# Performance work log

Measured on AMD Instinct MI355X. Metric: run time of the kernel, lower is better.

Reference implementation:

```python
import jax, jax.numpy as jnp
import numpy as np

# Multi-scale feature pyramid (static: determines per-level slice bounds)
SPATIAL_SHAPES = np.array([[100, 100], [50, 50], [25, 25], [13, 13], [7, 7]])  # (H, W) per level
LEVEL_START = np.concatenate([[0], np.cumsum(SPATIAL_SHAPES[:, 0] * SPATIAL_SHAPES[:, 1])])[:-1]
C = 256       # hidden_inplanes
HEADS = 8     # head_nums
POINTS = 4    # point_nums
LEVELS = 5    # feature_level_nums
FF = 2048     # feedforward_planes
DH = C // HEADS


def setup_inputs() -> dict:
    key = jax.random.key(0)
    ks = jax.random.split(key, 16)
    B = 2
    L = int((SPATIAL_SHAPES[:, 0] * SPATIAL_SHAPES[:, 1]).sum())  # 13343 tokens
    s = 0.02
    return {
        'src': jax.random.normal(ks[0], (B, L, C), jnp.float32),
        'pos': jax.random.normal(ks[1], (B, L, C), jnp.float32) * 0.1,
        'reference_points': jax.random.uniform(ks[2], (B, L, LEVELS, 2), jnp.float32),
        'wv': jax.random.normal(ks[3], (C, C), jnp.float32) * s,
        'bv': jnp.zeros((C,), jnp.float32),
        'wo': jax.random.normal(ks[4], (C, HEADS * LEVELS * POINTS * 2), jnp.float32) * s,
        'bo': jax.random.normal(ks[5], (HEADS * LEVELS * POINTS * 2,), jnp.float32) * 0.5,
        'wa': jax.random.normal(ks[6], (C, HEADS * LEVELS * POINTS), jnp.float32) * s,
        'ba': jnp.zeros((HEADS * LEVELS * POINTS,), jnp.float32),
        'wout': jax.random.normal(ks[7], (C, C), jnp.float32) * s,
        'bout': jnp.zeros((C,), jnp.float32),
        'ln1g': jnp.ones((C,), jnp.float32),
        'ln1b': jnp.zeros((C,), jnp.float32),
        'w1': jax.random.normal(ks[8], (C, FF), jnp.float32) * s,
        'b1': jnp.zeros((FF,), jnp.float32),
        'w2': jax.random.normal(ks[9], (FF, C), jnp.float32) * s,
        'b2': jnp.zeros((C,), jnp.float32),
        'ln2g': jnp.ones((C,), jnp.float32),
        'ln2b': jnp.zeros((C,), jnp.float32),
    }


def layernorm(x, g, b, eps=1e-5):
    m = jnp.mean(x, -1, keepdims=True)
    v = jnp.var(x, -1, keepdims=True)
    return (x - m) * jax.lax.rsqrt(v + eps) * g + b


def bilinear_sample(val, loc, Hs, Ws):
    # val: [B, heads, H*W, dh]   loc: [B, heads, Lq, P, 2] normalized coords in [0,1]
    # grid_sample semantics, align_corners=False, zero padding outside
    px = loc[..., 0] * Ws - 0.5
    py = loc[..., 1] * Hs - 0.5
    x0 = jnp.floor(px); y0 = jnp.floor(py)
    lx = px - x0;       ly = py - y0
    x0i = x0.astype(jnp.int32); y0i = y0.astype(jnp.int32)
    gather = jax.vmap(jax.vmap(lambda v, i: v[i]))  # over batch, head dims
    out = jnp.zeros(loc.shape[:-1] + (val.shape[-1],), val.dtype)
    for dx, dy, w in ((0, 0, (1 - lx) * (1 - ly)), (1, 0, lx * (1 - ly)),
                      (0, 1, (1 - lx) * ly), (1, 1, lx * ly)):
        xi = x0i + dx; yi = y0i + dy
        valid = (xi >= 0) & (xi < Ws) & (yi >= 0) & (yi < Hs)
        idx = jnp.clip(yi, 0, Hs - 1) * Ws + jnp.clip(xi, 0, Ws - 1)
        g = gather(val, idx)  # [B, heads, Lq, P, dh]
        out = out + (w * valid)[..., None] * g
    return out


def msdeform_attn(query, value_in, ref, wv, bv, wo, bo, wa, ba, wout, bout):
    B, Lq, _ = query.shape
    # value projection -> [B, heads, Len, dh]
    value = (value_in @ wv + bv).reshape(B, -1, HEADS, DH).transpose(0, 2, 1, 3)
    offsets = (query @ wo + bo).reshape(B, Lq, HEADS, LEVELS, POINTS, 2)
    attn = jax.nn.softmax((query @ wa + ba).reshape(B, Lq, HEADS, LEVELS * POINTS), -1)
    attn = attn.reshape(B, Lq, HEADS, LEVELS, POINTS)
    # offset normalizer = (W, H) per level
    norml = jnp.asarray(SPATIAL_SHAPES[:, ::-1].copy(), jnp.float32)
    loc = ref[:, :, None, :, None, :] + offsets / norml[None, None, None, :, None, :]
    acc = jnp.zeros((B, Lq, HEADS, DH), query.dtype)
    for l in range(LEVELS):
        Hs, Ws = int(SPATIAL_SHAPES[l, 0]), int(SPATIAL_SHAPES[l, 1])
        s = int(LEVEL_START[l])
        vl = value[:, :, s:s + Hs * Ws, :]
        locl = jnp.transpose(loc[:, :, :, l], (0, 2, 1, 3, 4))  # [B, heads, Lq, P, 2]
        samp = bilinear_sample(vl, locl, Hs, Ws)                 # [B, heads, Lq, P, dh]
        acc = acc + jnp.einsum('bhqpd,bqhp->bqhd', samp, attn[:, :, :, l])
    return acc.reshape(B, Lq, C) @ wout + bout


def reference(src, pos, reference_points, wv, bv, wo, bo, wa, ba, wout, bout,
              ln1g, ln1b, w1, b1, w2, b2, ln2g, ln2b):
    # DeformableTransformerEncoderLayer (eval mode, dropout off)
    q = src + pos
    src2 = msdeform_attn(q, src, reference_points, wv, bv, wo, bo, wa, ba, wout, bout)
    x = layernorm(src + src2, ln1g, ln1b)
    ffn = jax.nn.relu(x @ w1 + b1) @ w2 + b2
    return layernorm(x + ffn, ln2g, ln2b)
```

## Files before the change

### kernel.cpp

```cpp
#include <hip/hip_runtime.h>
#include <hip/hip_bf16.h>

typedef __hip_bfloat16 bf16;
typedef unsigned short ushort_t;
typedef __attribute__((ext_vector_type(8))) short bf16x8;
typedef __attribute__((ext_vector_type(16))) float f32x16;

__device__ __forceinline__ float us2f(unsigned short u) {
    unsigned int x = ((unsigned int)u) << 16;
    return __uint_as_float(x);
}
__device__ __forceinline__ ushort_t f2us(float f) {
    return ((__hip_bfloat16_raw)__float2bfloat16(f)).x;
}

__device__ __forceinline__ void gl_lds16(const ushort_t* g, ushort_t* l) {
    __builtin_amdgcn_global_load_lds(
        (const __attribute__((address_space(1))) void*)g,
        (__attribute__((address_space(3))) void*)l, 16, 0, 0);
}

__global__ __launch_bounds__(256) void cast2_kernel(
    const float* __restrict__ src, const float* __restrict__ pos,
    bf16* __restrict__ src_b, bf16* __restrict__ q_b, int n)
{
    int i = (blockIdx.x * 256 + threadIdx.x) * 4;
    if (i < n) {
        const float4 s4 = *reinterpret_cast<const float4*>(&src[i]);
        const float4 p4 = *reinterpret_cast<const float4*>(&pos[i]);
        int2 sp, qp;
        sp.x = (unsigned)f2us(s4.x) | ((unsigned)f2us(s4.y) << 16);
        sp.y = (unsigned)f2us(s4.z) | ((unsigned)f2us(s4.w) << 16);
        qp.x = (unsigned)f2us(s4.x + p4.x) | ((unsigned)f2us(s4.y + p4.y) << 16);
        qp.y = (unsigned)f2us(s4.z + p4.z) | ((unsigned)f2us(s4.w + p4.w) << 16);
        *reinterpret_cast<int2*>((ushort_t*)src_b + i) = sp;
        *reinterpret_cast<int2*>((ushort_t*)q_b + i) = qp;
    }
}

__global__ __launch_bounds__(256) void prep_kernel(
    const float* __restrict__ wv, const float* __restrict__ wo,
    const float* __restrict__ wa, const float* __restrict__ wout,
    const float* __restrict__ w1, const float* __restrict__ w2,
    const float* __restrict__ bo, const float* __restrict__ ba,
    bf16* __restrict__ wvt, bf16* __restrict__ wcat, bf16* __restrict__ woutt,
    bf16* __restrict__ w1t, bf16* __restrict__ w2t, float* __restrict__ bcat)
{
    __shared__ float tile[32][33];
    const int b = blockIdx.x;
    const float* W; bf16* Wt; int K, N, tb;
    if (b < 64)        { W = wv;   Wt = wvt;            K = 256;  N = 256;  tb = b; }
    else if (b < 144)  { W = wo;   Wt = wcat;           K = 256;  N = 320;  tb = b - 64; }
    else if (b < 184)  { W = wa;   Wt = wcat + 320*256; K = 256;  N = 160;  tb = b - 144; }
    else if (b < 248)  { W = wout; Wt = woutt;          K = 256;  N = 256;  tb = b - 184; }
    else if (b < 760)  { W = w1;   Wt = w1t;            K = 256;  N = 2048; tb = b - 248; }
    else if (b < 1272) { W = w2;   Wt = w2t;            K = 2048; N = 256;  tb = b - 760; }
    else {
        int i = (b - 1272) * 256 + threadIdx.x;
        if (i < 320) bcat[i] = bo[i];
        else if (i < 480) bcat[i] = ba[i - 320];
        return;
    }
    const int ntn = N >> 5;
    const int nb = (tb % ntn) * 32, kb = (tb / ntn) * 32;
    const int tx = threadIdx.x & 31, ty = threadIdx.x >> 5;
    #pragma unroll
    for (int i = 0; i < 32; i += 8) {
        int k = kb + ty + i, n = nb + tx;
        tile[ty + i][tx] = (k < K && n < N) ? W[(size_t)k * N + n] : 0.f;
    }
    __syncthreads();
    #pragma unroll
    for (int i = 0; i < 32; i += 8) {
        int n = nb + ty + i, k = kb + tx;
        if (n < N && k < K)
            Wt[(size_t)n * K + k] = __float2bfloat16(tile[tx][ty + i]);
    }
}

template<bool RELU, bool OUT_BF16, bool HAS_RESID, bool RESID_BF16, int NT, int WPE>
__global__ __launch_bounds__(256, WPE) void gemm_mfma_s(
    const ushort_t* __restrict__ A,
    const ushort_t* __restrict__ Bt,
    const float* __restrict__ bias,
    const void* __restrict__ residv,
    void* __restrict__ outv, int M, int N, int K, int mtiles)
{
    __shared__ ushort_t Asmem[64 * 32];
    __shared__ ushort_t Bsmem[128 * 32];
    const int lid = blockIdx.x;
    const int tbk = lid >> 3;
    const int xb = tbk & (NT - 1);
    const int yg = (tbk / NT) * 8 + (lid & 7);
    if (yg >= mtiles) return;
    const int m0 = yg * 64;
    const int n0 = xb * 128;

    const int tid = threadIdx.x;
    const int lane = tid & 63;
    const int wave = tid >> 6;
    const int l32 = lane & 31;
    const int hi  = lane >> 5;
    const int wm = wave >> 1;
    const int wn = wave & 1;

    const int srow = lane >> 2;
    const int sch  = (lane & 3) * 8;

    int mA = m0 + wave * 16 + srow; if (mA > M - 1) mA = M - 1;
    const ushort_t* aP = A + (size_t)mA * K + sch;
    ushort_t* aL = &Asmem[(wave * 16) * 32];
    const ushort_t* bP[2]; ushort_t* bL[2];
    #pragma unroll
    for (int i = 0; i < 2; ++i) {
        const int rbase = wave * 32 + i * 16;
        int nB = n0 + rbase + srow; if (nB > N - 1) nB = N - 1;
        bP[i] = Bt + (size_t)nB * K + sch;
        bL[i] = &Bsmem[rbase * 32];
    }

    f32x16 acc[2] = {};

    for (int k0 = 0; k0 < K; k0 += 32) {
        gl_lds16(aP, aL);       aP    += 32;
        gl_lds16(bP[0], bL[0]); bP[0] += 32;
        gl_lds16(bP[1], bL[1]); bP[1] += 32;
        __syncthreads();

        #pragma unroll
        for (int kw = 0; kw < 2; ++kw) {
            const bf16x8 af = *reinterpret_cast<const bf16x8*>(
                &Asmem[(wm * 32 + l32) * 32 + kw * 16 + hi * 8]);
            bf16x8 bfr[2];
            #pragma unroll
            for (int j = 0; j < 2; ++j) {
                const int rowB = wn * 64 + j * 32 + l32;
                bfr[j] = *reinterpret_cast<const bf16x8*>(
                    &Bsmem[rowB * 32 + kw * 16 + hi * 8]);
            }
            #pragma unroll
            for (int j = 0; j < 2; ++j)
                acc[j] = __builtin_amdgcn_mfma_f32_32x32x16_bf16(
                    af, bfr[j], acc[j], 0, 0, 0);
        }
        __syncthreads();
    }

    const int mb = m0 + wm * 32 + hi * 4;
    #pragma unroll
    for (int j = 0; j < 2; ++j) {
        const int n = n0 + wn * 64 + j * 32 + l32;
        if (n >= N) continue;
        const float bval = bias[n];
        #pragma unroll
        for (int r = 0; r < 16; ++r) {
            const int m = mb + (r & 3) + (r >> 2) * 8;
            if (m >= M) continue;
            float v = acc[j][r] + bval;
            if (HAS_RESID) {
                if (RESID_BF16)
                    v += us2f(((const ushort_t*)residv)[(size_t)m * N + n]);
                else
                    v += ((const float*)residv)[(size_t)m * N + n];
            }
            if (RELU) v = fmaxf(v, 0.f);
            if (OUT_BF16)
                ((bf16*)outv)[(size_t)m * N + n] = __float2bfloat16(v);
            else
                ((float*)outv)[(size_t)m * N + n] = v;
        }
    }
}

__global__ __launch_bounds__(256) void msda_kernel_v3(
    const ushort_t* __restrict__ og,
    const float* __restrict__ refp,
    const ushort_t* __restrict__ value,
    bf16* __restrict__ out,
    int M, int L)
{
    const int tid = threadIdx.x;
    const int qbase = blockIdx.x * 8;

    __shared__ float  s_attn[8][160];
    __shared__ int2   s_off[1280];
    __shared__ float4 s_w[1280];
    __shared__ int    s_Wl[5], s_St[5];

    if (tid < 5) {
        const int HW[5] = {100, 50, 25, 13, 7};
        const int st[5] = {0, 10000, 12500, 13125, 13294};
        s_Wl[tid] = HW[tid];
        s_St[tid] = st[tid];
    }

    for (int i = tid; i < 1280; i += 256) {
        int q = i / 160, j = i - q * 160;
        int qq = qbase + q;
        s_attn[q][j] = (qq < M) ? us2f(og[(size_t)qq * 480 + 320 + j]) : 0.f;
    }
    __syncthreads();

    if (tid < 64) {
        float* a = &s_attn[tid >> 3][(tid & 7) * 20];
        float mx = -1e30f;
        #pragma unroll
        for (int i = 0; i < 20; ++i) mx = fmaxf(mx, a[i]);
        float ssum = 0.f;
        #pragma unroll
        for (int i = 0; i < 20; ++i) {
            float e = __expf(a[i] - mx);
            a[i] = e;
            ssum += e;
        }
        float inv = 1.f / ssum;
        #pragma unroll
        for (int i = 0; i < 20; ++i) a[i] *= inv;
    }
    __syncthreads();

    #pragma unroll
    for (int it = 0; it < 5; ++it) {
        const int t = tid + it * 256;
        const int q  = t / 160;
        const int r  = t - q * 160;
        const int l  = (r - (r / 20) * 20) >> 2;
        const int qq = qbase + q;

        int2 offp = {0, 0};
        float4 wp = {0.f, 0.f, 0.f, 0.f};
        if (qq < M) {
            const int Wi = s_Wl[l];
            const int s0 = s_St[l];
            const float Wf = (float)Wi;
            const float ox = us2f(og[(size_t)qq * 480 + r * 2]);
            const float oy = us2f(og[(size_t)qq * 480 + r * 2 + 1]);
            const float2 rf = *reinterpret_cast<const float2*>(
                &refp[(size_t)qq * 10 + l * 2]);
            const float a = s_attn[q][r];

            const float px = fmaf(rf.x, Wf, -0.5f) + ox;
            const float py = fmaf(rf.y, Wf, -0.5f) + oy;
            const float x0f = floorf(px);
            const float y0f = floorf(py);
            const float lx = px - x0f;
            const float ly = py - y0f;
            const int x0 = (int)x0f;
            const int y0 = (int)y0f;

            const float wx0v = (x0 >= 0 && x0 < Wi) ? (1.f - lx) : 0.f;
            const float wx1v = (x0 + 1 >= 0 && x0 + 1 < Wi) ? lx : 0.f;
            const float wy0v = (y0 >= 0 && y0 < Wi) ? (1.f - ly) : 0.f;
            const float wy1v = (y0 + 1 >= 0 && y0 + 1 < Wi) ? ly : 0.f;

            const int c0 = min(max(x0, 0), Wi - 2);
            const int r0 = min(max(y0, 0), Wi - 2);
            const float swx0 = (x0 == c0 ? wx0v : 0.f) + (x0 + 1 == c0 ? wx1v : 0.f);
            const float swx1 = (x0 == c0 + 1 ? wx0v : 0.f) + (x0 + 1 == c0 + 1 ? wx1v : 0.f);
            const float swy0 = (y0 == r0 ? wy0v : 0.f) + (y0 + 1 == r0 ? wy1v : 0.f);
            const float swy1 = (y0 == r0 + 1 ? wy0v : 0.f) + (y0 + 1 == r0 + 1 ? wy1v : 0.f);

            offp.x = (s0 + r0 * Wi + c0) * 512;
            offp.y = offp.x + Wi * 512;
            wp.x = a * swx0 * swy0;
            wp.y = a * swx1 * swy0;
            wp.z = a * swx0 * swy1;
            wp.w = a * swx1 * swy1;
        }
        s_off[t] = offp;
        s_w[t] = wp;
    }
    __syncthreads();

    const int qi  = tid >> 5;
    const int g   = tid & 31;
    const int h   = g >> 2;
    const int sub = g & 3;
    const int bq = qbase + qi;
    if (bq >= M) return;
    const int b = bq / L;

    const char* vb = (const char*)value + (size_t)b * L * 512 + h * 64 + sub * 16;

    float acc[8] = {};
    const int tb = qi * 160 + h * 20;
    #pragma unroll 2
    for (int p = 0; p < 20; ++p) {
        const int2 off = s_off[tb + p];
        const float4 w = s_w[tb + p];
        const int4 u00 = *reinterpret_cast<const int4*>(vb + off.x);
        const int4 u10 = *reinterpret_cast<const int4*>(vb + off.x + 512);
        const int4 u01 = *reinterpret_cast<const int4*>(vb + off.y);
        const int4 u11 = *reinterpret_cast<const int4*>(vb + off.y + 512);
        #define ACC4(u, wt)                                                        \
            acc[0] = fmaf(wt, __uint_as_float((unsigned)(u).x << 16), acc[0]);      \
            acc[1] = fmaf(wt, __uint_as_float((unsigned)(u).x & 0xffff0000u), acc[1]); \
            acc[2] = fmaf(wt, __uint_as_float((unsigned)(u).y << 16), acc[2]);      \
            acc[3] = fmaf(wt, __uint_as_float((unsigned)(u).y & 0xffff0000u), acc[3]); \
            acc[4] = fmaf(wt, __uint_as_float((unsigned)(u).z << 16), acc[4]);      \
            acc[5] = fmaf(wt, __uint_as_float((unsigned)(u).z & 0xffff0000u), acc[5]); \
            acc[6] = fmaf(wt, __uint_as_float((unsigned)(u).w << 16), acc[6]);      \
            acc[7] = fmaf(wt, __uint_as_float((unsigned)(u).w & 0xffff0000u), acc[7]);
        ACC4(u00, w.x)
        ACC4(u10, w.y)
        ACC4(u01, w.z)
        ACC4(u11, w.w)
        #undef ACC4
    }

    ushort_t o[8];
    #pragma unroll
    for (int i = 0; i < 8; ++i) o[i] = f2us(acc[i]);
    int4 pkt;
    pkt.x = (int)o[0] | ((int)o[1] << 16);
    pkt.y = (int)o[2] | ((int)o[3] << 16);
    pkt.z = (int)o[4] | ((int)o[5] << 16);
    pkt.w = (int)o[6] | ((int)o[7] << 16);
    *reinterpret_cast<int4*>((ushort_t*)out + (size_t)bq * 256 + h * 32 + sub * 8) = pkt;
}

template<bool OUT_BF16>
__global__ __launch_bounds__(256) void ln_kernel(
    const ushort_t* __restrict__ yb, const float* __restrict__ g,
    const float* __restrict__ bta, void* __restrict__ outv, int M)
{
    const int wave = threadIdx.x >> 6, lane = threadIdx.x & 63;
    const int row = blockIdx.x * 4 + wave;
    if (row >= M) return;
    const int2 raw = *reinterpret_cast<const int2*>(&yb[(size_t)row * 256 + lane * 4]);
    float v0 = us2f((ushort_t)((unsigned)raw.x & 0xffffu));
    float v1 = us2f((ushort_t)((unsigned)raw.x >> 16));
    float v2 = us2f((ushort_t)((unsigned)raw.y & 0xffffu));
    float v3 = us2f((ushort_t)((unsigned)raw.y >> 16));
    float s  = v0 + v1 + v2 + v3;
    float ss = v0 * v0 + v1 * v1 + v2 * v2 + v3 * v3;
    #pragma unroll
    for (int o = 32; o > 0; o >>= 1) {
        s += __shfl_down(s, o);
        ss += __shfl_down(ss, o);
    }
    s = __shfl(s, 0);
    ss = __shfl(ss, 0);
    const float mean = s * (1.f / 256.f);
    const float var = ss * (1.f / 256.f) - mean * mean;
    const float rs = rsqrtf(var + 1e-5f);
    const float4 g4 = *reinterpret_cast<const float4*>(&g[lane * 4]);
    const float4 b4 = *reinterpret_cast<const float4*>(&bta[lane * 4]);
    float4 o4;
    o4.x = (v0 - mean) * rs * g4.x + b4.x;
    o4.y = (v1 - mean) * rs * g4.y + b4.y;
    o4.z = (v2 - mean) * rs * g4.z + b4.z;
    o4.w = (v3 - mean) * rs * g4.w + b4.w;
    if (OUT_BF16) {
        int2 pk;
        pk.x = (unsigned)f2us(o4.x) | ((unsigned)f2us(o4.y) << 16);
        pk.y = (unsigned)f2us(o4.z) | ((unsigned)f2us(o4.w) << 16);
        *reinterpret_cast<int2*>((ushort_t*)outv + (size_t)row * 256 + lane * 4) = pk;
    } else {
        *reinterpret_cast<float4*>((float*)outv + (size_t)row * 256 + lane * 4) = o4;
    }
}

extern "C" void kernel_launch(void* const* d_in, const int* in_sizes, int n_in,
                              void* d_out, int out_size, void* d_ws, size_t ws_size,
                              hipStream_t stream)
{
    const int B = 2, L = 13343, C = 256, FF = 2048;
    const int M = B * L;

    const float* src  = (const float*)d_in[0];
    const float* pos  = (const float*)d_in[1];
    const float* refp = (const float*)d_in[2];
    const float* wv   = (const float*)d_in[3];
    const float* bv   = (const float*)d_in[4];
    const float* wo   = (const float*)d_in[5];
    const float* bo   = (const float*)d_in[6];
    const float* wa   = (const float*)d_in[7];
    const float* ba   = (const float*)d_in[8];
    const float* wout = (const float*)d_in[9];
    const float* bout = (const float*)d_in[10];
    const float* ln1g = (const float*)d_in[11];
    const float* ln1b = (const float*)d_in[12];
    const float* w1   = (const float*)d_in[13];
    const float* b1   = (const float*)d_in[14];
    const float* w2   = (const float*)d_in[15];
    const float* b2   = (const float*)d_in[16];
    const float* ln2g = (const float*)d_in[17];
    const float* ln2b = (const float*)d_in[18];

    char* ws = (char*)d_ws;
    const size_t MB = 1ull << 20;
    bf16*  src_b  = (bf16*)(ws + 0);
    bf16*  q_b    = (bf16*)(ws + 14 * MB);
    bf16*  val_b  = (bf16*)(ws + 28 * MB);
    bf16*  og     = (bf16*)(ws + 42 * MB);
    bf16*  acc_b  = (bf16*)(ws + 95 * MB);
    bf16*  h_b    = (bf16*)(ws + 0);
    bf16*  y      = (bf16*)(ws + 110 * MB);
    bf16*  z      = (bf16*)(ws + 110 * MB);
    bf16*  x_b    = (bf16*)(ws + 138 * MB);
    bf16* wvt    = (bf16*)(ws + 152 * MB);
    bf16* wcat   = wvt + 256 * 256;
    bf16* woutt  = wcat + 480 * 256;
    bf16* w1t    = woutt + 256 * 256;
    bf16* w2t    = w1t + 2048 * 256;
    float* bcat  = (float*)(w2t + 256 * 2048);
    (void)ws_size; (void)n_in; (void)in_sizes; (void)out_size;

    const int mt64 = (M + 63) / 64;
    const int gm8  = (mt64 + 7) / 8;
    const int lnb  = (M + 3) / 4;

    prep_kernel<<<1274, 256, 0, stream>>>(wv, wo, wa, wout, w1, w2, bo, ba,
                                          wvt, wcat, woutt, w1t, w2t, bcat);

    cast2_kernel<<<(M * C / 4 + 255) / 256, 256, 0, stream>>>(
        src, pos, src_b, q_b, M * C);

    gemm_mfma_s<false, true, false, false, 2, 4><<<gm8 * 16, 256, 0, stream>>>(
        (const ushort_t*)src_b, (const ushort_t*)wvt, bv, nullptr, val_b,
        M, 256, 256, mt64);

    gemm_mfma_s<false, true, false, false, 4, 8><<<gm8 * 32, 256, 0, stream>>>(
        (const ushort_t*)q_b, (const ushort_t*)wcat, bcat, nullptr, og,
        M, 480, 256, mt64);

    msda_kernel_v3<<<(M + 7) / 8, 256, 0, stream>>>(
        (const ushort_t*)og, refp, (const ushort_t*)val_b, acc_b, M, L);

    gemm_mfma_s<false, true, true, false, 2, 4><<<gm8 * 16, 256, 0, stream>>>(
        (const ushort_t*)acc_b, (const ushort_t*)woutt, bout, src, y,
        M, 256, 256, mt64);

    ln_kernel<true><<<lnb, 256, 0, stream>>>(
        (const ushort_t*)y, ln1g, ln1b, x_b, M);

    gemm_mfma_s<true, true, false, false, 16, 8><<<gm8 * 128, 256, 0, stream>>>(
        (const ushort_t*)x_b, (const ushort_t*)w1t, b1, nullptr, h_b,
        M, FF, 256, mt64);

    gemm_mfma_s<false, true, true, true, 2, 4><<<gm8 * 16, 256, 0, stream>>>(
        (const ushort_t*)h_b, (const ushort_t*)w2t, b2, x_b, z,
        M, 256, FF, mt64);

    ln_kernel<false><<<lnb, 256, 0, stream>>>(
        (const ushort_t*)z, ln2g, ln2b, (float*)d_out, M);
}
```

Measured before the change: 389.3 us.

## Swizzle GEMM shared-memory layout and stage epilogue through LDS for vector stores

Reorganizes the bf16 GEMM's LDS tiles into an XOR-swizzled layout and precomputes the per-lane read pointers, aiming to remove bank conflicts on the MFMA operand reads. The epilogue now stages the accumulators through a shared float buffer so each thread writes four contiguous outputs and reads the residual with vector loads, replacing scattered scalar stores. Two launches have their waves-per-EU hint lowered from 8 to 4 to fit the larger shared footprint. The cost is extra syncs and LDS traffic in the epilogue, plus possibly lower occupancy. Columns are written only in groups of four, so a tail group that does not fill four columns would be skipped.

```diff
diff --git a/kernel.cpp b/kernel.cpp
--- a/kernel.cpp
+++ b/kernel.cpp
@@ -86,8 +86,11 @@
     const void* __restrict__ residv,
     void* __restrict__ outv, int M, int N, int K, int mtiles)
 {
-    __shared__ ushort_t Asmem[64 * 32];
-    __shared__ ushort_t Bsmem[128 * 32];
+    __shared__ __align__(16) char smemraw[17408];
+    ushort_t* Asmem = (ushort_t*)smemraw;
+    ushort_t* Bsmem = (ushort_t*)(smemraw + 4096);
+    float (*epi)[68] = (float(*)[68])smemraw;
+
     const int lid = blockIdx.x;
     const int tbk = lid >> 3;
     const int xb = tbk & (NT - 1);
@@ -104,19 +107,45 @@
     const int wm = wave >> 1;
     const int wn = wave & 1;
 
-    const int srow = lane >> 2;
-    const int sch  = (lane & 3) * 8;
-
-    int mA = m0 + wave * 16 + srow; if (mA > M - 1) mA = M - 1;
-    const ushort_t* aP = A + (size_t)mA * K + sch;
-    ushort_t* aL = &Asmem[(wave * 16) * 32];
+    const int lsup = lane >> 3;
+    const int clin = lane & 7;
+
+    const int gsA = wave * 8 + lsup;
+    const int csA = clin ^ (gsA & 7);
+    int rA = m0 + gsA * 2 + (csA >> 2); if (rA > M - 1) rA = M - 1;
+    const ushort_t* aP = A + (size_t)rA * K + (csA & 3) * 8;
+    ushort_t* aL = Asmem + wave * 512;
+
     const ushort_t* bP[2]; ushort_t* bL[2];
     #pragma unroll
     for (int i = 0; i < 2; ++i) {
-        const int rbase = wave * 32 + i * 16;
-        int nB = n0 + rbase + srow; if (nB > N - 1) nB = N - 1;
-        bP[i] = Bt + (size_t)nB * K + sch;
-        bL[i] = &Bsmem[rbase * 32];
+        const int gsB = wave * 16 + i * 8 + lsup;
+        const int csB = clin ^ (gsB & 7);
+        int rB = n0 + gsB * 2 + (csB >> 2); if (rB > N - 1) rB = N - 1;
+        bP[i] = Bt + (size_t)rB * K + (csB & 3) * 8;
+        bL[i] = Bsmem + (wave * 16 + i * 8) * 64;
+    }
+
+    const int arow = wm * 32 + l32;
+    const int asup = arow >> 1;
+    const ushort_t* aR[2];
+    #pragma unroll
+    for (int kw = 0; kw < 2; ++kw) {
+        const int q = kw * 2 + hi;
+        const int slot = (((arow & 1) << 2) | q) ^ (asup & 7);
+        aR[kw] = Asmem + asup * 64 + slot * 8;
+    }
+    const ushort_t* bR[2][2];
+    #pragma unroll
+    for (int j = 0; j < 2; ++j) {
+        const int brow = wn * 64 + j * 32 + l32;
+        const int bsup = brow >> 1;
+        #pragma unroll
+        for (int kw = 0; kw < 2; ++kw) {
+            const int q = kw * 2 + hi;
+            const int slot = (((brow & 1) << 2) | q) ^ (bsup & 7);
+            bR[j][kw] = Bsmem + bsup * 64 + slot * 8;
+        }
     }
 
     f32x16 acc[2] = {};
@@ -129,46 +158,69 @@
 
         #pragma unroll
         for (int kw = 0; kw < 2; ++kw) {
-            const bf16x8 af = *reinterpret_cast<const bf16x8*>(
-                &Asmem[(wm * 32 + l32) * 32 + kw * 16 + hi * 8]);
-            bf16x8 bfr[2];
-            #pragma unroll
-            for (int j = 0; j < 2; ++j) {
-                const int rowB = wn * 64 + j * 32 + l32;
-                bfr[j] = *reinterpret_cast<const bf16x8*>(
-                    &Bsmem[rowB * 32 + kw * 16 + hi * 8]);
-            }
+            const bf16x8 af = *reinterpret_cast<const bf16x8*>(aR[kw]);
             #pragma unroll
             for (int j = 0; j < 2; ++j)
                 acc[j] = __builtin_amdgcn_mfma_f32_32x32x16_bf16(
-                    af, bfr[j], acc[j], 0, 0, 0);
+                    af, *reinterpret_cast<const bf16x8*>(bR[j][kw]), acc[j], 0, 0, 0);
         }
         __syncthreads();
     }
 
-    const int mb = m0 + wm * 32 + hi * 4;
-    #pragma unroll
-    for (int j = 0; j < 2; ++j) {
-        const int n = n0 + wn * 64 + j * 32 + l32;
-        if (n >= N) continue;
-        const float bval = bias[n];
+    #pragma unroll
+    for (int half = 0; half < 2; ++half) {
+        if (wn == half) {
+            #pragma unroll
+            for (int j = 0; j < 2; ++j) {
+                const int coll = j * 32 + l32;
+                const int n = n0 + half * 64 + coll;
+                const float bv = (n < N) ? bias[n] : 0.f;
+                #pragma unroll
+                for (int r = 0; r < 16; ++r) {
+                    const int row = wm * 32 + hi * 4 + (r & 3) + (r >> 2) * 8;
+                    epi[row][coll] = acc[j][r] + bv;
+                }
+            }
+        }
+        __syncthreads();
         #pragma unroll
-        for (int r = 0; r < 16; ++r) {
-            const int m = mb + (r & 3) + (r >> 2) * 8;
-            if (m >= M) continue;
-            float v = acc[j][r] + bval;
-            if (HAS_RESID) {
-                if (RESID_BF16)
-                    v += us2f(((const ushort_t*)residv)[(size_t)m * N + n]);
-                else
-                    v += ((const float*)residv)[(size_t)m * N + n];
+        for (int i = 0; i < 4; ++i) {
+            const int idx = i * 256 + tid;
+            const int row = idx >> 4;
+            const int c4  = idx & 15;
+            const int m = m0 + row;
+            const int n = n0 + half * 64 + c4 * 4;
+            if (m < M && n + 3 < N) {
+                float4 v = *reinterpret_cast<const float4*>(&epi[row][c4 * 4]);
+                if (HAS_RESID) {
+                    if (RESID_BF16) {
+                        const int2 rw = *reinterpret_cast<const int2*>(
+                            (const ushort_t*)residv + (size_t)m * N + n);
+                        v.x += us2f((ushort_t)((unsigned)rw.x & 0xffffu));
+                        v.y += us2f((ushort_t)((unsigned)rw.x >> 16));
+                        v.z += us2f((ushort_t)((unsigned)rw.y & 0xffffu));
+                        v.w += us2f((ushort_t)((unsigned)rw.y >> 16));
+                    } else {
+                        const float4 r4 = *reinterpret_cast<const float4*>(
+                            (const float*)residv + (size_t)m * N + n);
+                        v.x += r4.x; v.y += r4.y; v.z += r4.z; v.w += r4.w;
+                    }
+                }
+                if (RELU) {
+                    v.x = fmaxf(v.x, 0.f); v.y = fmaxf(v.y, 0.f);
+                    v.z = fmaxf(v.z, 0.f); v.w = fmaxf(v.w, 0.f);
+                }
+                if (OUT_BF16) {
+                    int2 pk;
+                    pk.x = (unsigned)f2us(v.x) | ((unsigned)f2us(v.y) << 16);
+                    pk.y = (unsigned)f2us(v.z) | ((unsigned)f2us(v.w) << 16);
+                    *reinterpret_cast<int2*>((ushort_t*)outv + (size_t)m * N + n) = pk;
+                } else {
+                    *reinterpret_cast<float4*>((float*)outv + (size_t)m * N + n) = v;
+                }
             }
-            if (RELU) v = fmaxf(v, 0.f);
-            if (OUT_BF16)
-                ((bf16*)outv)[(size_t)m * N + n] = __float2bfloat16(v);
-            else
-                ((float*)outv)[(size_t)m * N + n] = v;
         }
+        if (half == 0) __syncthreads();
     }
 }
 
@@ -421,7 +473,7 @@
         (const ushort_t*)src_b, (const ushort_t*)wvt, bv, nullptr, val_b,
         M, 256, 256, mt64);
 
-    gemm_mfma_s<false, true, false, false, 4, 8><<<gm8 * 32, 256, 0, stream>>>(
+    gemm_mfma_s<false, true, false, false, 4, 4><<<gm8 * 32, 256, 0, stream>>>(
         (const ushort_t*)q_b, (const ushort_t*)wcat, bcat, nullptr, og,
         M, 480, 256, mt64);
 
@@ -435,7 +487,7 @@
     ln_kernel<true><<<lnb, 256, 0, stream>>>(
         (const ushort_t*)y, ln1g, ln1b, x_b, M);
 
-    gemm_mfma_s<true, true, false, false, 16, 8><<<gm8 * 128, 256, 0, stream>>>(
+    gemm_mfma_s<true, true, false, false, 16, 4><<<gm8 * 128, 256, 0, stream>>>(
         (const ushort_t*)x_b, (const ushort_t*)w1t, b1, nullptr, h_b,
         M, FF, 256, mt64);
 
```

Result: faster. 365.0 us (-6.2%).
